# Optimization experiments

Hardware: AMD Instinct MI355X
Metric: run time of the kernel (lower is better)

Reference implementation:

```python
import jax, jax.numpy as jnp
import numpy as np

TOP_K = 2


def setup_inputs() -> dict:
    key = jax.random.key(0)
    ks = jax.random.split(key, 5)
    B, S, D, F, E = 2, 1024, 1024, 4096, 8
    return {
        "hidden_states": jax.random.normal(ks[0], (B, S, D), jnp.float32),
        "gate_w": jax.random.normal(ks[1], (E, D), jnp.float32) * 0.02,
        "w1": jax.random.normal(ks[2], (E, D, F), jnp.float32) * 0.02,
        "w2": jax.random.normal(ks[3], (E, F, D), jnp.float32) * 0.02,
        "w3": jax.random.normal(ks[4], (E, D, F), jnp.float32) * 0.02,
    }


def reference(hidden_states, gate_w, w1, w2, w3):
    B, S, D = hidden_states.shape
    E = gate_w.shape[0]
    x = hidden_states.reshape(-1, D).astype(jnp.float32)  # [T, D]
    T = x.shape[0]

    # Router: softmax over experts, top-k, renormalize selected weights.
    router_logits = x @ gate_w.T                      # [T, E]
    probs = jax.nn.softmax(router_logits, axis=-1)
    top_w, top_e = jax.lax.top_k(probs, TOP_K)        # [T, K]
    top_w = top_w / jnp.sum(top_w, axis=-1, keepdims=True)

    # Combine weights [T, E]: weight of expert e for token t (0 if not selected).
    combine = jnp.zeros((T, E), jnp.float32).at[jnp.arange(T)[:, None], top_e].add(top_w)

    # Expert SwiGLU FFNs (vectorized over experts; unselected contributions are
    # zeroed by combine weights, matching the gather/scatter math exactly).
    h = jnp.einsum('td,edf->etf', x, w1)              # [E, T, F]
    g = jnp.einsum('td,edf->etf', x, w3)              # [E, T, F]
    y = jnp.einsum('etf,efd->etd', jax.nn.silu(h) * g, w2)  # [E, T, D]

    out = jnp.einsum('etd,te->td', y, combine)        # weighted scatter-combine
    return out.reshape(B, S, D), router_logits
```

## Files before the change

### kernel.cpp

```cpp
#include <hip/hip_runtime.h>
#include <hip/hip_bf16.h>
#include <math.h>

#define T_TOK   2048
#define DDIM    1024
#define FDIM    4096
#define NEXP    8
#define MAXROWS 4608

typedef __bf16          bf16x8 __attribute__((ext_vector_type(8)));
typedef float           f32x4  __attribute__((ext_vector_type(4)));
typedef unsigned short  u16x8  __attribute__((ext_vector_type(8)));

#define LDSP 40
#define FCW  128

static __device__ __forceinline__ unsigned short f2b(float f) {
    __hip_bfloat16 h = __float2bfloat16(f);
    return __builtin_bit_cast(unsigned short, h);
}

static __device__ __forceinline__ void gll16(const unsigned short* g, unsigned short* l) {
    __builtin_amdgcn_global_load_lds(
        (const __attribute__((address_space(1))) unsigned int*)g,
        (__attribute__((address_space(3))) unsigned int*)l, 16, 0, 0);
}

__global__ __launch_bounds__(256) void moe_router_kernel(
    const float* __restrict__ x, const float* __restrict__ gate_w,
    float* __restrict__ logits_out, int* __restrict__ top_e, float* __restrict__ top_w)
{
    int wid  = (blockIdx.x * blockDim.x + threadIdx.x) >> 6;
    int lane = threadIdx.x & 63;
    if (wid >= T_TOK) return;
    const float* xr = x + (size_t)wid * DDIM;
    float acc[NEXP];
    #pragma unroll
    for (int e = 0; e < NEXP; ++e) acc[e] = 0.f;
    for (int d = lane; d < DDIM; d += 64) {
        float xv = xr[d];
        #pragma unroll
        for (int e = 0; e < NEXP; ++e) acc[e] += xv * gate_w[e * DDIM + d];
    }
    #pragma unroll
    for (int e = 0; e < NEXP; ++e) {
        #pragma unroll
        for (int off = 32; off > 0; off >>= 1)
            acc[e] += __shfl_down(acc[e], off, 64);
    }
    if (lane == 0) {
        #pragma unroll
        for (int e = 0; e < NEXP; ++e) logits_out[wid * NEXP + e] = acc[e];
        int e1 = 0;
        #pragma unroll
        for (int e = 1; e < NEXP; ++e) if (acc[e] > acc[e1]) e1 = e;
        int e2 = (e1 == 0) ? 1 : 0;
        #pragma unroll
        for (int e = 0; e < NEXP; ++e) if (e != e1 && acc[e] > acc[e2]) e2 = e;
        float p2 = __expf(acc[e2] - acc[e1]);
        float s  = 1.0f + p2;
        top_e[wid * 2]     = e1;
        top_e[wid * 2 + 1] = e2;
        top_w[wid * 2]     = 1.0f / s;
        top_w[wid * 2 + 1] = p2 / s;
    }
}

__global__ void moe_scatter_kernel(const int* __restrict__ top_e, const float* __restrict__ top_w,
                                   int* __restrict__ cnt, int* __restrict__ list_tok,
                                   float* __restrict__ list_w)
{
    int t = blockIdx.x * blockDim.x + threadIdx.x;
    if (t >= T_TOK) return;
    #pragma unroll
    for (int s = 0; s < 2; ++s) {
        int e   = top_e[t * 2 + s];
        int pos = atomicAdd(&cnt[e], 1);
        list_tok[e * T_TOK + pos] = t;
        list_w [e * T_TOK + pos] = top_w[t * 2 + s];
    }
}

__global__ void moe_prefix_kernel(const int* __restrict__ cnt, int* __restrict__ offs)
{
    if (threadIdx.x == 0 && blockIdx.x == 0) {
        int o = 0;
        #pragma unroll
        for (int e = 0; e < NEXP; ++e) { offs[e] = o; o += ((cnt[e] + 63) >> 6) << 6; }
        offs[NEXP] = o;
    }
}

__global__ __launch_bounds__(256) void transpose_cvt2_kernel(
    const float* __restrict__ srcA, unsigned short* __restrict__ dstA,
    const float* __restrict__ srcB, unsigned short* __restrict__ dstB, int R, int C)
{
    int tilesC = C >> 6;
    int tilesPerMat = (R >> 6) * tilesC;
    int e  = blockIdx.x / tilesPerMat;
    int t  = blockIdx.x - e * tilesPerMat;
    int tr = t / tilesC, tc = t - tr * tilesC;
    size_t soff = (size_t)e * R * C + (size_t)(tr * 64) * C + tc * 64;
    size_t doff = (size_t)e * R * C + (size_t)(tc * 64) * R + tr * 64;

    __shared__ unsigned short lds[64][72];
    int tid = threadIdx.x;
    int rr = tid >> 4, cc = (tid & 15) * 4;
    int orow = tid >> 2, oc = (tid & 3) * 16;

    #pragma unroll
    for (int m = 0; m < 2; ++m) {
        const float*    s = (m == 0 ? srcA : srcB) + soff;
        unsigned short* d = (m == 0 ? dstA : dstB) + doff;
        if (m) __syncthreads();
        #pragma unroll
        for (int i = 0; i < 4; ++i) {
            int r = rr + 16 * i;
            float4 v = *(const float4*)(s + (size_t)r * C + cc);
            lds[cc + 0][r] = f2b(v.x); lds[cc + 1][r] = f2b(v.y);
            lds[cc + 2][r] = f2b(v.z); lds[cc + 3][r] = f2b(v.w);
        }
        __syncthreads();
        u16x8 a = *(const u16x8*)&lds[orow][oc];
        u16x8 b = *(const u16x8*)&lds[orow][oc + 8];
        *(u16x8*)(d + (size_t)orow * R + oc)     = a;
        *(u16x8*)(d + (size_t)orow * R + oc + 8) = b;
    }
}

__global__ __launch_bounds__(256) void transpose_cvt_kernel(
    const float* __restrict__ src, unsigned short* __restrict__ dst, int R, int C)
{
    int tilesC = C >> 6;
    int tilesPerMat = (R >> 6) * tilesC;
    int e  = blockIdx.x / tilesPerMat;
    int t  = blockIdx.x - e * tilesPerMat;
    int tr = t / tilesC, tc = t - tr * tilesC;
    const float*    s = src + (size_t)e * R * C + (size_t)(tr * 64) * C + tc * 64;
    unsigned short* d = dst + (size_t)e * R * C + (size_t)(tc * 64) * R + tr * 64;

    __shared__ unsigned short lds[64][72];
    int tid = threadIdx.x;
    int rr = tid >> 4, cc = (tid & 15) * 4;
    #pragma unroll
    for (int i = 0; i < 4; ++i) {
        int r = rr + 16 * i;
        float4 v = *(const float4*)(s + (size_t)r * C + cc);
        lds[cc + 0][r] = f2b(v.x); lds[cc + 1][r] = f2b(v.y);
        lds[cc + 2][r] = f2b(v.z); lds[cc + 3][r] = f2b(v.w);
    }
    __syncthreads();
    int orow = tid >> 2, oc = (tid & 3) * 16;
    u16x8 a = *(const u16x8*)&lds[orow][oc];
    u16x8 b = *(const u16x8*)&lds[orow][oc + 8];
    *(u16x8*)(d + (size_t)orow * R + oc)     = a;
    *(u16x8*)(d + (size_t)orow * R + oc + 8) = b;
}

__global__ __launch_bounds__(256) void moe_gather_kernel(
    const float* __restrict__ x, const int* __restrict__ list_tok,
    const int* __restrict__ cnt, const int* __restrict__ offs,
    unsigned short* __restrict__ xg)
{
    int e  = blockIdx.x >> 8;
    int rb = blockIdx.x & 255;
    int n = cnt[e];
    int npad = (n + 63) & ~63;
    if (rb * 8 >= npad) return;
    int base = offs[e];
    int tid = threadIdx.x;
    #pragma unroll
    for (int i = 0; i < 4; ++i) {
        int u = tid + 256 * i;
        int r = u >> 7, cu = u & 127;
        int slot = rb * 8 + r;
        int tok = list_tok[e * T_TOK + slot];
        const float* sp = x + (size_t)tok * DDIM + cu * 8;
        float4 v0 = *(const float4*)(sp);
        float4 v1 = *(const float4*)(sp + 4);
        u16x8 t8;
        t8[0]=f2b(v0.x); t8[1]=f2b(v0.y); t8[2]=f2b(v0.z); t8[3]=f2b(v0.w);
        t8[4]=f2b(v1.x); t8[5]=f2b(v1.y); t8[6]=f2b(v1.z); t8[7]=f2b(v1.w);
        *(u16x8*)(xg + (size_t)(base + slot) * DDIM + cu * 8) = t8;
    }
}

__global__ __launch_bounds__(256, 2) void moe_up_kernel(
    const unsigned short* __restrict__ xg,
    const unsigned short* __restrict__ w1t, const unsigned short* __restrict__ w3t,
    const int* __restrict__ cnt, const int* __restrict__ offs,
    unsigned short* __restrict__ act)
{
    int e   = blockIdx.x & 7;
    int idx = blockIdx.x >> 3;
    int mt  = idx >> 5;
    int fc  = idx & 31;
    int n = cnt[e];
    int npad = (n + 63) & ~63;
    if (mt * 128 >= npad) return;
    int rowBase  = offs[e] + mt * 128;
    int rowMax   = offs[e] + npad - 1;
    int rowLimit = offs[e] + npad;

    __shared__ unsigned short As [128 * 32];
    __shared__ unsigned short B1s[128 * 32];
    __shared__ unsigned short B2s[128 * 32];

    int tid = threadIdx.x;
    int lane = tid & 63, wv = tid >> 6;
    int c = lane & 15, g = lane >> 4;
    int wr = (wv >> 1) * 64, wc = (wv & 1) * 64;

    int srow = tid >> 2, skc = tid & 3;
    int r0 = min(rowBase + srow,      rowMax);
    int r1 = min(rowBase + 64 + srow, rowMax);
    const unsigned short* gA0 = xg + (size_t)r0 * DDIM + skc * 8;
    const unsigned short* gA1 = xg + (size_t)r1 * DDIM + skc * 8;
    size_t wb = (size_t)e * FDIM * DDIM + (size_t)(fc * 128 + srow) * DDIM + skc * 8;
    const unsigned short* gB1a = w1t + wb;
    const unsigned short* gB1b = w1t + wb + (size_t)64 * DDIM;
    const unsigned short* gB2a = w3t + wb;
    const unsigned short* gB2b = w3t + wb + (size_t)64 * DDIM;
    unsigned short* lA0  = As  + tid * 8;
    unsigned short* lA1  = As  + 2048 + tid * 8;
    unsigned short* lB1a = B1s + tid * 8;
    unsigned short* lB1b = B1s + 2048 + tid * 8;
    unsigned short* lB2a = B2s + tid * 8;
    unsigned short* lB2b = B2s + 2048 + tid * 8;

    f32x4 acc_h[4][4], acc_g[4][4];
    #pragma unroll
    for (int i = 0; i < 4; ++i)
        #pragma unroll
        for (int j = 0; j < 4; ++j) { acc_h[i][j] = (f32x4)(0.f); acc_g[i][j] = (f32x4)(0.f); }

    for (int k0 = 0; k0 < DDIM; k0 += 32) {
        gll16(gA0  + k0, lA0);
        gll16(gA1  + k0, lA1);
        gll16(gB1a + k0, lB1a);
        gll16(gB1b + k0, lB1b);
        gll16(gB2a + k0, lB2a);
        gll16(gB2b + k0, lB2b);
        __syncthreads();

        bf16x8 af[4];
        #pragma unroll
        for (int mi = 0; mi < 4; ++mi)
            af[mi] = *reinterpret_cast<const bf16x8*>(&As[(wr + mi * 16 + c) * 32 + g * 8]);
        #pragma unroll
        for (int ni = 0; ni < 4; ++ni) {
            bf16x8 b1 = *reinterpret_cast<const bf16x8*>(&B1s[(wc + ni * 16 + c) * 32 + g * 8]);
            bf16x8 b2 = *reinterpret_cast<const bf16x8*>(&B2s[(wc + ni * 16 + c) * 32 + g * 8]);
            #pragma unroll
            for (int mi = 0; mi < 4; ++mi) {
                acc_h[mi][ni] = __builtin_amdgcn_mfma_f32_16x16x32_bf16(af[mi], b1, acc_h[mi][ni], 0, 0, 0);
                acc_g[mi][ni] = __builtin_amdgcn_mfma_f32_16x16x32_bf16(af[mi], b2, acc_g[mi][ni], 0, 0, 0);
            }
        }
        __syncthreads();
    }

    #pragma unroll
    for (int mi = 0; mi < 4; ++mi) {
        int row = rowBase + wr + mi * 16 + 4 * g;
        if (row < rowLimit) {
            #pragma unroll
            for (int ni = 0; ni < 4; ++ni) {
                int col = fc * 128 + wc + ni * 16 + c;
                #pragma unroll
                for (int r = 0; r < 4; ++r) {
                    float h  = acc_h[mi][ni][r];
                    float gg = acc_g[mi][ni][r];
                    float a  = h / (1.f + __expf(-h)) * gg;
                    act[(size_t)(row + r) * FDIM + col] = f2b(a);
                }
            }
        }
    }
}

__global__ __launch_bounds__(256, 3) void moe_down_kernel(
    const unsigned short* __restrict__ act, const unsigned short* __restrict__ w2t,
    const int* __restrict__ cnt, const int* __restrict__ offs,
    const int* __restrict__ list_tok, const float* __restrict__ list_w,
    float* __restrict__ out)
{
    int e   = blockIdx.x & 7;
    int idx = blockIdx.x >> 3;
    int mt  = idx >> 5;
    int ks  = (idx >> 3) & 3;
    int dc  = idx & 7;
    int n = cnt[e];
    int npad = (n + 63) & ~63;
    if (mt * 128 >= npad) return;
    int rowBase = offs[e] + mt * 128;
    int rowMax  = offs[e] + npad - 1;

    __shared__ unsigned short As[128 * 32];
    __shared__ unsigned short Bs[128 * 32];

    int tid = threadIdx.x;
    int lane = tid & 63, wv = tid >> 6;
    int c = lane & 15, g = lane >> 4;
    int wr = (wv >> 1) * 64, wc = (wv & 1) * 64;

    int srow = tid >> 2, skc = tid & 3;
    int r0 = min(rowBase + srow,      rowMax);
    int r1 = min(rowBase + 64 + srow, rowMax);
    const unsigned short* gA0 = act + (size_t)r0 * FDIM + ks * 1024 + skc * 8;
    const unsigned short* gA1 = act + (size_t)r1 * FDIM + ks * 1024 + skc * 8;
    size_t wb = (size_t)e * DDIM * FDIM + (size_t)(dc * 128 + srow) * FDIM + ks * 1024 + skc * 8;
    const unsigned short* gBa = w2t + wb;
    const unsigned short* gBb = w2t + wb + (size_t)64 * FDIM;
    unsigned short* lA0 = As + tid * 8;
    unsigned short* lA1 = As + 2048 + tid * 8;
    unsigned short* lBa = Bs + tid * 8;
    unsigned short* lBb = Bs + 2048 + tid * 8;

    f32x4 acc[4][4];
    #pragma unroll
    for (int i = 0; i < 4; ++i)
        #pragma unroll
        for (int j = 0; j < 4; ++j) acc[i][j] = (f32x4)(0.f);

    for (int k0 = 0; k0 < 1024; k0 += 32) {
        gll16(gA0 + k0, lA0);
        gll16(gA1 + k0, lA1);
        gll16(gBa + k0, lBa);
        gll16(gBb + k0, lBb);
        __syncthreads();

        bf16x8 af[4];
        #pragma unroll
        for (int mi = 0; mi < 4; ++mi)
            af[mi] = *reinterpret_cast<const bf16x8*>(&As[(wr + mi * 16 + c) * 32 + g * 8]);
        #pragma unroll
        for (int ni = 0; ni < 4; ++ni) {
            bf16x8 b = *reinterpret_cast<const bf16x8*>(&Bs[(wc + ni * 16 + c) * 32 + g * 8]);
            #pragma unroll
            for (int mi = 0; mi < 4; ++mi)
                acc[mi][ni] = __builtin_amdgcn_mfma_f32_16x16x32_bf16(af[mi], b, acc[mi][ni], 0, 0, 0);
        }
        __syncthreads();
    }

    #pragma unroll
    for (int mi = 0; mi < 4; ++mi) {
        #pragma unroll
        for (int r = 0; r < 4; ++r) {
            int s = mt * 128 + wr + mi * 16 + 4 * g + r;
            if (s < n) {
                int   tok = list_tok[e * T_TOK + s];
                float wt  = list_w [e * T_TOK + s];
                #pragma unroll
                for (int ni = 0; ni < 4; ++ni) {
                    int col = dc * 128 + wc + ni * 16 + c;
                    atomicAdd(&out[(size_t)tok * DDIM + col], wt * acc[mi][ni][r]);
                }
            }
        }
    }
}

__global__ __launch_bounds__(256, 3) void moe_up_legacy(
    const float* __restrict__ x, const float* __restrict__ w1, const float* __restrict__ w3,
    const int* __restrict__ cnt, const int* __restrict__ offs,
    const int* __restrict__ list_tok, unsigned short* __restrict__ act)
{
    const int NWG = NEXP * 32 * 32;
    int bid     = blockIdx.x;
    int logical = (bid & 7) * (NWG >> 3) + (bid >> 3);
    int tile = logical & 31;
    int fc   = (logical >> 5) & 31;
    int e    = logical >> 10;
    int n = cnt[e];
    if (tile * 64 >= n) return;

    __shared__ unsigned short As [64  * LDSP];
    __shared__ unsigned short B1s[FCW * LDSP];
    __shared__ unsigned short B2s[FCW * LDSP];

    int tid = threadIdx.x;
    int lane = tid & 63, wv = tid >> 6;
    int c = lane & 15, g = lane >> 4;
    int ar = tid >> 2, akq = tid & 3;
    int tok = list_tok[e * T_TOK + tile * 64 + ar];
    const float* xrow = x + (size_t)tok * DDIM + akq * 8;
    int bcol = tid & 127, bkh = tid >> 7;
    const size_t wbase = (size_t)e * DDIM * FDIM + (size_t)fc * FCW + bcol;
    const float* w1c = w1 + wbase;
    const float* w3c = w3 + wbase;

    f32x4 acc_h[4][2], acc_g[4][2];
    #pragma unroll
    for (int i = 0; i < 4; ++i)
        #pragma unroll
        for (int j = 0; j < 2; ++j) { acc_h[i][j] = (f32x4)(0.f); acc_g[i][j] = (f32x4)(0.f); }

    for (int k0 = 0; k0 < DDIM; k0 += 32) {
        {
            const float4 v0 = *(const float4*)(xrow + k0);
            const float4 v1 = *(const float4*)(xrow + k0 + 4);
            u16x8 t8;
            t8[0]=f2b(v0.x); t8[1]=f2b(v0.y); t8[2]=f2b(v0.z); t8[3]=f2b(v0.w);
            t8[4]=f2b(v1.x); t8[5]=f2b(v1.y); t8[6]=f2b(v1.z); t8[7]=f2b(v1.w);
            *reinterpret_cast<u16x8*>(&As[ar * LDSP + akq * 8]) = t8;
        }
        {
            int kb = k0 + bkh * 16;
            u16x8 t1a, t1b, t2a, t2b;
            #pragma unroll
            for (int j = 0; j < 8; ++j) {
                t1a[j] = f2b(w1c[(size_t)(kb + j)     * FDIM]);
                t1b[j] = f2b(w1c[(size_t)(kb + 8 + j) * FDIM]);
                t2a[j] = f2b(w3c[(size_t)(kb + j)     * FDIM]);
                t2b[j] = f2b(w3c[(size_t)(kb + 8 + j) * FDIM]);
            }
            *reinterpret_cast<u16x8*>(&B1s[bcol * LDSP + bkh * 16])     = t1a;
            *reinterpret_cast<u16x8*>(&B1s[bcol * LDSP + bkh * 16 + 8]) = t1b;
            *reinterpret_cast<u16x8*>(&B2s[bcol * LDSP + bkh * 16])     = t2a;
            *reinterpret_cast<u16x8*>(&B2s[bcol * LDSP + bkh * 16 + 8]) = t2b;
        }
        __syncthreads();
        bf16x8 af[4];
        #pragma unroll
        for (int mi = 0; mi < 4; ++mi)
            af[mi] = *reinterpret_cast<const bf16x8*>(&As[(mi * 16 + c) * LDSP + g * 8]);
        #pragma unroll
        for (int ni = 0; ni < 2; ++ni) {
            int col = wv * 32 + ni * 16 + c;
            bf16x8 b1 = *reinterpret_cast<const bf16x8*>(&B1s[col * LDSP + g * 8]);
            bf16x8 b2 = *reinterpret_cast<const bf16x8*>(&B2s[col * LDSP + g * 8]);
            #pragma unroll
            for (int mi = 0; mi < 4; ++mi) {
                acc_h[mi][ni] = __builtin_amdgcn_mfma_f32_16x16x32_bf16(af[mi], b1, acc_h[mi][ni], 0, 0, 0);
                acc_g[mi][ni] = __builtin_amdgcn_mfma_f32_16x16x32_bf16(af[mi], b2, acc_g[mi][ni], 0, 0, 0);
            }
        }
        __syncthreads();
    }
    int rowBase = offs[e] + tile * 64;
    #pragma unroll
    for (int mi = 0; mi < 4; ++mi)
        #pragma unroll
        for (int ni = 0; ni < 2; ++ni)
            #pragma unroll
            for (int r = 0; r < 4; ++r) {
                float h  = acc_h[mi][ni][r];
                float gg = acc_g[mi][ni][r];
                float a  = h / (1.f + __expf(-h)) * gg;
                int row = rowBase + mi * 16 + 4 * g + r;
                int col = fc * FCW + wv * 32 + ni * 16 + c;
                act[(size_t)row * FDIM + col] = f2b(a);
            }
}

__global__ __launch_bounds__(256, 3) void moe_down_legacy(
    const unsigned short* __restrict__ act, const float* __restrict__ w2,
    const int* __restrict__ cnt, const int* __restrict__ offs,
    const int* __restrict__ list_tok, const float* __restrict__ list_w,
    float* __restrict__ out)
{
    const int NWG = NEXP * 4 * 4 * 32;
    int bid     = blockIdx.x;
    int logical = (bid & 7) * (NWG >> 3) + (bid >> 3);
    int tile = logical & 31;
    int ks   = (logical >> 5) & 3;
    int dc   = (logical >> 7) & 3;
    int e    = logical >> 9;
    int n = cnt[e];
    if (tile * 64 >= n) return;

    __shared__ unsigned short As[64  * LDSP];
    __shared__ unsigned short Bs[256 * LDSP];
    int tid = threadIdx.x;
    int lane = tid & 63, wv = tid >> 6;
    int c = lane & 15, g = lane >> 4;
    int rowBase = offs[e] + tile * 64;
    int ar = tid >> 2, akq = tid & 3;
    const unsigned short* arow = act + (size_t)(rowBase + ar) * FDIM + ks * 1024 + akq * 8;
    const float* w2c = w2 + (size_t)e * FDIM * DDIM + (size_t)(ks * 1024) * DDIM + (size_t)dc * 256 + tid;

    f32x4 acc[4][4];
    #pragma unroll
    for (int i = 0; i < 4; ++i)
        #pragma unroll
        for (int j = 0; j < 4; ++j) acc[i][j] = (f32x4)(0.f);

    for (int k0 = 0; k0 < 1024; k0 += 32) {
        *reinterpret_cast<u16x8*>(&As[ar * LDSP + akq * 8]) = *reinterpret_cast<const u16x8*>(arow + k0);
        #pragma unroll
        for (int kk = 0; kk < 4; ++kk) {
            u16x8 t1;
            #pragma unroll
            for (int j = 0; j < 8; ++j)
                t1[j] = f2b(w2c[(size_t)(k0 + kk * 8 + j) * DDIM]);
            *reinterpret_cast<u16x8*>(&Bs[tid * LDSP + kk * 8]) = t1;
        }
        __syncthreads();
        bf16x8 af[4];
        #pragma unroll
        for (int mi = 0; mi < 4; ++mi)
            af[mi] = *reinterpret_cast<const bf16x8*>(&As[(mi * 16 + c) * LDSP + g * 8]);
        #pragma unroll
        for (int ni = 0; ni < 4; ++ni) {
            bf16x8 b = *reinterpret_cast<const bf16x8*>(&Bs[(wv * 64 + ni * 16 + c) * LDSP + g * 8]);
            #pragma unroll
            for (int mi = 0; mi < 4; ++mi)
                acc[mi][ni] = __builtin_amdgcn_mfma_f32_16x16x32_bf16(af[mi], b, acc[mi][ni], 0, 0, 0);
        }
        __syncthreads();
    }
    #pragma unroll
    for (int mi = 0; mi < 4; ++mi)
        #pragma unroll
        for (int r = 0; r < 4; ++r) {
            int s = tile * 64 + mi * 16 + 4 * g + r;
            if (s < n) {
                int   tok = list_tok[e * T_TOK + s];
                float wt  = list_w [e * T_TOK + s];
                #pragma unroll
                for (int ni = 0; ni < 4; ++ni) {
                    int col = dc * 256 + wv * 64 + ni * 16 + c;
                    atomicAdd(&out[(size_t)tok * DDIM + col], wt * acc[mi][ni][r]);
                }
            }
        }
}

extern "C" void kernel_launch(void* const* d_in, const int* in_sizes, int n_in,
                              void* d_out, int out_size, void* d_ws, size_t ws_size,
                              hipStream_t stream) {
    const float* x      = (const float*)d_in[0];
    const float* gate_w = (const float*)d_in[1];
    const float* w1     = (const float*)d_in[2];
    const float* w2     = (const float*)d_in[3];
    const float* w3     = (const float*)d_in[4];
    float* out        = (float*)d_out;
    float* logits_out = out + (size_t)T_TOK * DDIM;

    char* ws = (char*)d_ws;
    int*   cnt      = (int*)  (ws);
    int*   offs     = (int*)  (ws + 64);
    int*   top_e    = (int*)  (ws + 1024);
    float* top_w    = (float*)(ws + 17408);
    int*   list_tok = (int*)  (ws + 33792);
    float* list_w   = (float*)(ws + 99328);

    hipMemsetAsync(cnt, 0, 64, stream);
    hipMemsetAsync(list_tok, 0, 131072, stream);
    hipMemsetAsync(out, 0, (size_t)T_TOK * DDIM * sizeof(float), stream);

    moe_router_kernel <<<T_TOK / 4,   256, 0, stream>>>(x, gate_w, logits_out, top_e, top_w);
    moe_scatter_kernel<<<T_TOK / 256, 256, 0, stream>>>(top_e, top_w, cnt, list_tok, list_w);
    moe_prefix_kernel <<<1, 64, 0, stream>>>(cnt, offs);

    const size_t MB = 1u << 20;
    const size_t NEED = 241 * MB;
    if (ws_size >= NEED) {
        unsigned short* xg  = (unsigned short*)(ws + 1   * MB);
        unsigned short* act = (unsigned short*)(ws + 11  * MB);
        unsigned short* w1t = (unsigned short*)(ws + 49  * MB);
        unsigned short* w3t = (unsigned short*)(ws + 113 * MB);
        unsigned short* w2t = (unsigned short*)(ws + 177 * MB);

        moe_gather_kernel<<<NEXP * 256, 256, 0, stream>>>(x, list_tok, cnt, offs, xg);
        transpose_cvt2_kernel<<<NEXP * 16 * 64, 256, 0, stream>>>(w1, w1t, w3, w3t, DDIM, FDIM);
        transpose_cvt_kernel <<<NEXP * 64 * 16, 256, 0, stream>>>(w2, w2t, FDIM, DDIM);

        moe_up_kernel   <<<NEXP * 16 * 32, 256, 0, stream>>>(xg, w1t, w3t, cnt, offs, act);
        moe_down_kernel <<<NEXP * 16 * 32, 256, 0, stream>>>(act, w2t, cnt, offs, list_tok, list_w, out);
    } else {
        unsigned short* act = (unsigned short*)(ws + 164864);
        moe_up_legacy   <<<NEXP * 32 * 32,    256, 0, stream>>>(x, w1, w3, cnt, offs, list_tok, act);
        moe_down_legacy <<<NEXP * 4 * 4 * 32, 256, 0, stream>>>(act, w2, cnt, offs, list_tok, list_w, out);
    }
}
```

Measured before the change: 397.0 us.

## Double-buffer LDS tiles in MoE up and down GEMM kernels

Both expert GEMM kernels now hold two LDS buffers per operand. The global-to-LDS loads for the next K-slice are issued before the MFMA work on the current slice, so memory latency can overlap with compute. Each iteration now ends with a single barrier that serves both buffers. The cost is double the shared memory per block, which could reduce occupancy, and the overlap depends on how the compiler places the waitcnt for the async LDS loads.

After: 417.7 us. +5.2%, slower.

```diff
diff --git a/kernel.cpp b/kernel.cpp
--- a/kernel.cpp
+++ b/kernel.cpp
@@ -202,9 +202,9 @@
     int rowMax   = offs[e] + npad - 1;
     int rowLimit = offs[e] + npad;
 
-    __shared__ unsigned short As [128 * 32];
-    __shared__ unsigned short B1s[128 * 32];
-    __shared__ unsigned short B2s[128 * 32];
+    __shared__ unsigned short As [2][128 * 32];
+    __shared__ unsigned short B1s[2][128 * 32];
+    __shared__ unsigned short B2s[2][128 * 32];
 
     int tid = threadIdx.x;
     int lane = tid & 63, wv = tid >> 6;
@@ -221,12 +221,15 @@
     const unsigned short* gB1b = w1t + wb + (size_t)64 * DDIM;
     const unsigned short* gB2a = w3t + wb;
     const unsigned short* gB2b = w3t + wb + (size_t)64 * DDIM;
-    unsigned short* lA0  = As  + tid * 8;
-    unsigned short* lA1  = As  + 2048 + tid * 8;
-    unsigned short* lB1a = B1s + tid * 8;
-    unsigned short* lB1b = B1s + 2048 + tid * 8;
-    unsigned short* lB2a = B2s + tid * 8;
-    unsigned short* lB2b = B2s + 2048 + tid * 8;
+
+    auto STAGE = [&](int buf, int k0) {
+        gll16(gA0  + k0, &As [buf][tid * 8]);
+        gll16(gA1  + k0, &As [buf][2048 + tid * 8]);
+        gll16(gB1a + k0, &B1s[buf][tid * 8]);
+        gll16(gB1b + k0, &B1s[buf][2048 + tid * 8]);
+        gll16(gB2a + k0, &B2s[buf][tid * 8]);
+        gll16(gB2b + k0, &B2s[buf][2048 + tid * 8]);
+    };
 
     f32x4 acc_h[4][4], acc_g[4][4];
     #pragma unroll
@@ -234,23 +237,21 @@
         #pragma unroll
         for (int j = 0; j < 4; ++j) { acc_h[i][j] = (f32x4)(0.f); acc_g[i][j] = (f32x4)(0.f); }
 
-    for (int k0 = 0; k0 < DDIM; k0 += 32) {
-        gll16(gA0  + k0, lA0);
-        gll16(gA1  + k0, lA1);
-        gll16(gB1a + k0, lB1a);
-        gll16(gB1b + k0, lB1b);
-        gll16(gB2a + k0, lB2a);
-        gll16(gB2b + k0, lB2b);
-        __syncthreads();
+    STAGE(0, 0);
+    __syncthreads();
+
+    for (int t = 0; t < 32; ++t) {
+        int cur = t & 1;
+        if (t < 31) STAGE(cur ^ 1, (t + 1) * 32);
 
         bf16x8 af[4];
         #pragma unroll
         for (int mi = 0; mi < 4; ++mi)
-            af[mi] = *reinterpret_cast<const bf16x8*>(&As[(wr + mi * 16 + c) * 32 + g * 8]);
+            af[mi] = *reinterpret_cast<const bf16x8*>(&As[cur][(wr + mi * 16 + c) * 32 + g * 8]);
         #pragma unroll
         for (int ni = 0; ni < 4; ++ni) {
-            bf16x8 b1 = *reinterpret_cast<const bf16x8*>(&B1s[(wc + ni * 16 + c) * 32 + g * 8]);
-            bf16x8 b2 = *reinterpret_cast<const bf16x8*>(&B2s[(wc + ni * 16 + c) * 32 + g * 8]);
+            bf16x8 b1 = *reinterpret_cast<const bf16x8*>(&B1s[cur][(wc + ni * 16 + c) * 32 + g * 8]);
+            bf16x8 b2 = *reinterpret_cast<const bf16x8*>(&B2s[cur][(wc + ni * 16 + c) * 32 + g * 8]);
             #pragma unroll
             for (int mi = 0; mi < 4; ++mi) {
                 acc_h[mi][ni] = __builtin_amdgcn_mfma_f32_16x16x32_bf16(af[mi], b1, acc_h[mi][ni], 0, 0, 0);
@@ -296,8 +297,8 @@
     int rowBase = offs[e] + mt * 128;
     int rowMax  = offs[e] + npad - 1;
 
-    __shared__ unsigned short As[128 * 32];
-    __shared__ unsigned short Bs[128 * 32];
+    __shared__ unsigned short As[2][128 * 32];
+    __shared__ unsigned short Bs[2][128 * 32];
 
     int tid = threadIdx.x;
     int lane = tid & 63, wv = tid >> 6;
@@ -312,10 +313,13 @@
     size_t wb = (size_t)e * DDIM * FDIM + (size_t)(dc * 128 + srow) * FDIM + ks * 1024 + skc * 8;
     const unsigned short* gBa = w2t + wb;
     const unsigned short* gBb = w2t + wb + (size_t)64 * FDIM;
-    unsigned short* lA0 = As + tid * 8;
-    unsigned short* lA1 = As + 2048 + tid * 8;
-    unsigned short* lBa = Bs + tid * 8;
-    unsigned short* lBb = Bs + 2048 + tid * 8;
+
+    auto STAGE = [&](int buf, int k0) {
+        gll16(gA0 + k0, &As[buf][tid * 8]);
+        gll16(gA1 + k0, &As[buf][2048 + tid * 8]);
+        gll16(gBa + k0, &Bs[buf][tid * 8]);
+        gll16(gBb + k0, &Bs[buf][2048 + tid * 8]);
+    };
 
     f32x4 acc[4][4];
     #pragma unroll
@@ -323,20 +327,20 @@
         #pragma unroll
         for (int j = 0; j < 4; ++j) acc[i][j] = (f32x4)(0.f);
 
-    for (int k0 = 0; k0 < 1024; k0 += 32) {
-        gll16(gA0 + k0, lA0);
-        gll16(gA1 + k0, lA1);
-        gll16(gBa + k0, lBa);
-        gll16(gBb + k0, lBb);
-        __syncthreads();
+    STAGE(0, 0);
+    __syncthreads();
+
+    for (int t = 0; t < 32; ++t) {
+        int cur = t & 1;
+        if (t < 31) STAGE(cur ^ 1, (t + 1) * 32);
 
         bf16x8 af[4];
         #pragma unroll
         for (int mi = 0; mi < 4; ++mi)
-            af[mi] = *reinterpret_cast<const bf16x8*>(&As[(wr + mi * 16 + c) * 32 + g * 8]);
+            af[mi] = *reinterpret_cast<const bf16x8*>(&As[cur][(wr + mi * 16 + c) * 32 + g * 8]);
         #pragma unroll
         for (int ni = 0; ni < 4; ++ni) {
-            bf16x8 b = *reinterpret_cast<const bf16x8*>(&Bs[(wc + ni * 16 + c) * 32 + g * 8]);
+            bf16x8 b = *reinterpret_cast<const bf16x8*>(&Bs[cur][(wc + ni * 16 + c) * 32 + g * 8]);
             #pragma unroll
             for (int mi = 0; mi < 4; ++mi)
                 acc[mi][ni] = __builtin_amdgcn_mfma_f32_16x16x32_bf16(af[mi], b, acc[mi][ni], 0, 0, 0);
```
